# Kernel tuning notes

Measured on AMD Instinct MI355X. Metric: run time of the kernel, lower is better.

## Reference

```python
import jax, jax.numpy as jnp
import numpy as np

B, N, D, K = 4, 2048, 128, 32
EPS = 1e-5  # nn.LayerNorm default eps


def _lin(k, fan_in, fan_out):
    kw, kb = jax.random.split(k)
    s = 1.0 / np.sqrt(fan_in)
    w = jax.random.uniform(kw, (fan_in, fan_out), jnp.float32, -s, s)
    b = jax.random.uniform(kb, (fan_out,), jnp.float32, -s, s)
    return w, b


def setup_inputs() -> dict:
    key = jax.random.key(0)
    ks = jax.random.split(key, 3)
    inp = {}
    inp["features"] = jax.random.normal(ks[0], (B, N, D), jnp.float32)
    inp["coords"] = jax.random.uniform(ks[1], (B, N, 3), jnp.float32) * 64.0
    names = [("ql", D, D), ("kl", D, D), ("vl", D, D), ("pl1", 3, D), ("pl2", D, D),
             ("we1", D, D), ("we2", D, D), ("pe1", 3, D), ("pe2", D, D),
             ("sg1", D, D), ("sg2", D, D)]
    k2 = jax.random.split(ks[2], len(names))
    for (nm, fi, fo), kk in zip(names, k2):
        w, b = _lin(kk, fi, fo)
        inp[nm + "_w"] = w
        inp[nm + "_b"] = b
    inp["lnA_g"] = jnp.ones((D,), jnp.float32)
    inp["lnA_b"] = jnp.zeros((D,), jnp.float32)
    inp["lnF_g"] = jnp.ones((D,), jnp.float32)
    inp["lnF_b"] = jnp.zeros((D,), jnp.float32)
    return inp


def _sparsemax_k(z):
    # sparsemax over axis=1 (the K neighbor axis) of [N, K, D]
    zs = -jnp.sort(-z, axis=1)                      # descending sort
    zc = jnp.cumsum(zs, axis=1)
    r = jnp.arange(1, K + 1, dtype=z.dtype)[None, :, None]
    support = (r * zs) > (zc - 1.0)
    kz = jnp.sum(support, axis=1, keepdims=True).astype(jnp.int32)  # >= 1
    tau = (jnp.take_along_axis(zc, kz - 1, axis=1) - 1.0) / kz.astype(z.dtype)
    return jnp.maximum(z - tau, 0.0)


def _sg_prop(x, src, tgt, n):
    # SGConv (K=1) propagation: D^{-1/2}(A+I)D^{-1/2} x with self-loops added
    ar = jnp.arange(n)
    s = jnp.concatenate([src, ar])
    t = jnp.concatenate([tgt, ar])
    deg = jax.ops.segment_sum(jnp.ones(s.shape, x.dtype), t, num_segments=n)
    dinv = jax.lax.rsqrt(deg)
    norm = dinv[s] * dinv[t]
    return jax.ops.segment_sum(x[s] * norm[:, None], t, num_segments=n)


def reference(features, coords,
              ql_w, ql_b, kl_w, kl_b, vl_w, vl_b,
              pl1_w, pl1_b, pl2_w, pl2_b,
              we1_w, we1_b, we2_w, we2_b,
              lnA_g, lnA_b,
              pe1_w, pe1_b, pe2_w, pe2_b,
              sg1_w, sg1_b, sg2_w, sg2_b,
              lnF_g, lnF_b):
    def ln(x, g, b):
        m = jnp.mean(x, axis=-1, keepdims=True)
        v = jnp.var(x, axis=-1, keepdims=True)
        return (x - m) * jax.lax.rsqrt(v + EPS) * g + b

    def one(feat, coord):
        # ---- RNSA: KNN self-attention with positional embedding ----
        d2 = jnp.sum((coord[:, None, :] - coord[None, :, :]) ** 2, axis=-1)  # [N,N]
        _, idx = jax.lax.top_k(-d2, K)                   # [N,K], self included first
        diff = coord[idx] - coord[:, None, :]            # [N,K,3]
        fc = jnp.maximum(diff @ pl1_w + pl1_b, 0.0) @ pl2_w + pl2_b  # [N,K,D]
        pe = fc + feat[idx]
        Q = jnp.maximum(feat @ ql_w + ql_b, 0.0)         # [N,D]
        Kf = jnp.maximum(pe @ kl_w + kl_b, 0.0)          # [N,K,D]
        V = pe @ vl_w + vl_b
        rel = (Kf - Q[:, None, :]) * fc
        w = jnp.maximum(rel @ we1_w + we1_b, 0.0) @ we2_w + we2_b
        w = _sparsemax_k(w)                              # attn_drop is identity (eval)
        x_att = feat + jnp.einsum('nkd,nkd->nd', V, w)   # residual add
        cf = jnp.maximum(coord @ pe1_w + pe1_b, 0.0) @ pe2_w + pe2_b
        x_in = ln(x_att, lnA_g, lnA_b)
        x_pe = x_in + cf
        d2m = d2 + jnp.where(jnp.eye(N, dtype=bool), jnp.inf, 0.0)  # knn_graph: loop=False
        _, idx2 = jax.lax.top_k(-d2m, K)                 # [N,K] neighbors (sources)
        src = idx2.reshape(-1)
        tgt = jnp.repeat(jnp.arange(N), K)
        h = _sg_prop(x_pe, src, tgt, N) @ sg1_w + sg1_b
        h = jnp.maximum(h, 0.0)
        h = _sg_prop(h, src, tgt, N) @ sg2_w + sg2_b     # dropout is identity (eval)
        return ln(h + x_in, lnF_g, lnF_b)

    return jax.vmap(one)(features, coords)
```

## Files before the change

### kernel.cpp

```cpp
#include <hip/hip_runtime.h>
#include <hip/hip_bf16.h>


namespace {
constexpr int BB = 4;
constexpr int NN = 2048;
constexpr int DD = 128;
constexpr int KK = 32;
constexpr float LNEPS = 1e-5f;
constexpr int SH = 136;
constexpr int SF = 132;

constexpr int W_QL = 0, W_KL = 16384, W_VL = 32768, W_PL2 = 49152, W_WE1 = 65536,
              W_WE2 = 81920, W_PE2 = 98304, W_SG1 = 114688, W_SG2 = 131072,
              W_PL1 = 147456, W_PE1 = 147840,
              B_QL = 148224, B_KL = 148352, B_VL = 148480, B_PL1 = 148608, B_PL2 = 148736,
              B_WE1 = 148864, B_WE2 = 148992, B_PE1 = 149120, B_PE2 = 149248,
              B_SG1 = 149376, B_SG2 = 149504,
              LNA_G = 149632, LNA_B = 149760, LNF_G = 149888, LNF_B = 150016;

constexpr long OFF_FEAT  = 0;
constexpr long OFF_Q     = 1l << 20;
constexpr long OFF_XATT  = 2l << 20;
constexpr long OFF_XIN   = 3l << 20;
constexpr long OFF_XPE   = 4l << 20;
constexpr long OFF_H1    = 5l << 20;
constexpr long OFF_COORD = 6l << 20;
constexpr long OFF_W     = (6l << 20) + 32768;
constexpr long OFF_IDX   = (6l << 20) + 262144;
}

typedef _Float16 f16;
typedef __attribute__((ext_vector_type(8))) _Float16 half8;
typedef __attribute__((ext_vector_type(4))) float f32x4;

struct WPtrs { const void* p[26]; };

__device__ __forceinline__ f32x4 mfma16h(half8 a, half8 b, f32x4 c) {
  return __builtin_amdgcn_mfma_f32_16x16x32_f16(a, b, c, 0, 0, 0);
}
__device__ __forceinline__ bool bf_inputs(const unsigned* __restrict__ dt) {
  return (dt[0] & 0xFFFFu) != 0u;
}

__global__ __launch_bounds__(256) void k_prep(WPtrs wp,
    const void* __restrict__ feat, const void* __restrict__ coord,
    const unsigned* __restrict__ dt,
    float* __restrict__ featf, float* __restrict__ coordf, float* __restrict__ Wf,
    f16* __restrict__ pkH, f16* __restrict__ pkL) {
  const bool isbf = bf_inputs(dt);
  const int tid = threadIdx.x;
  if (blockIdx.x < 2048) {
    const int nf = BB * NN * DD, nc = BB * NN * 3;
    for (int i = blockIdx.x * 256 + tid; i < nf + nc; i += 2048 * 256) {
      if (i < nf) {
        featf[i] = isbf ? __bfloat162float(((const __hip_bfloat16*)feat)[i])
                        : ((const float*)feat)[i];
      } else {
        const int j = i - nf;
        coordf[j] = isbf ? __bfloat162float(((const __hip_bfloat16*)coord)[j])
                         : ((const float*)coord)[j];
      }
    }
  } else if (blockIdx.x < 2048 + 26) {
    const int sizes[26] = {16384,16384,16384,16384,16384,16384,16384,16384,16384,
                           384,384,
                           128,128,128,128,128,128,128,128,128,128,128,
                           128,128,128,128};
    const int offs[26] = {W_QL,W_KL,W_VL,W_PL2,W_WE1,W_WE2,W_PE2,W_SG1,W_SG2,
                          W_PL1,W_PE1,
                          B_QL,B_KL,B_VL,B_PL1,B_PL2,B_WE1,B_WE2,B_PE1,B_PE2,B_SG1,B_SG2,
                          LNA_G,LNA_B,LNF_G,LNF_B};
    const int t = blockIdx.x - 2048;
    float* dst = Wf + offs[t];
    const int n = sizes[t];
    if (isbf) {
      const __hip_bfloat16* src = (const __hip_bfloat16*)wp.p[t];
      for (int i = tid; i < n; i += 256) dst[i] = __bfloat162float(src[i]);
    } else {
      const float* src = (const float*)wp.p[t];
      for (int i = tid; i < n; i += 256) dst[i] = src[i];
    }
  } else {
    const int wmap[9] = {3, 1, 2, 4, 5, 6, 7, 8, 0};
    const int m = blockIdx.x - 2048 - 26;
    const void* src = wp.p[wmap[m]];
    f16* H = pkH + m * 16384;
    f16* L = pkL + m * 16384;
    for (int f = tid; f < 16384; f += 256) {
      const int j = f & 7, lane = (f >> 3) & 63, ks = (f >> 9) & 3, nt = f >> 11;
      const int k = ks * 32 + ((lane >> 4) << 3) + j, n = nt * 16 + (lane & 15);
      const float v = isbf ? __bfloat162float(((const __hip_bfloat16*)src)[k * 128 + n])
                           : ((const float*)src)[k * 128 + n];
      const f16 h = (f16)v;
      H[f] = h;
      L[f] = (f16)(v - (float)h);
    }
  }
}

__device__ __forceinline__ void mm_core(const f16* sA,
                                        const f16* __restrict__ wH,
                                        const f16* __restrict__ wL,
                                        bool useLoW, int lane, int wv, f32x4 acc[2][2]) {
  const int colq = lane & 15, quad = lane >> 4;
  #pragma unroll
  for (int mt = 0; mt < 2; ++mt) {
    const int arow = mt * 16 + colq;
    f32x4 a0 = {0.f, 0.f, 0.f, 0.f}, a1 = {0.f, 0.f, 0.f, 0.f};
    #pragma unroll
    for (int ks = 0; ks < 4; ++ks) {
      const half8 a = *(const half8*)(sA + arow * SH + ks * 32 + quad * 8);
      const int nt0 = 2 * wv, nt1 = 2 * wv + 1;
      const half8 b0 = *(const half8*)(wH + ((nt0 * 4 + ks) * 64 + lane) * 8);
      const half8 b1 = *(const half8*)(wH + ((nt1 * 4 + ks) * 64 + lane) * 8);
      a0 = mfma16h(a, b0, a0);
      a1 = mfma16h(a, b1, a1);
      if (useLoW) {
        const half8 bl0 = *(const half8*)(wL + ((nt0 * 4 + ks) * 64 + lane) * 8);
        const half8 bl1 = *(const half8*)(wL + ((nt1 * 4 + ks) * 64 + lane) * 8);
        a0 = mfma16h(a, bl0, a0);
        a1 = mfma16h(a, bl1, a1);
      }
    }
    acc[mt][0] = a0;
    acc[mt][1] = a1;
  }
}

__device__ __forceinline__ void h_store2(f16* A, int row0, int col, float v0, float v1) {
  A[row0 * SH + col] = (f16)v0;
  A[(row0 + 1) * SH + col] = (f16)v1;
}

__device__ __forceinline__ void h_store_row16(f16* A, int row, int c0, const float* v) {
  half8 o0, o1;
  #pragma unroll
  for (int e = 0; e < 8; ++e) { o0[e] = (f16)v[e]; o1[e] = (f16)v[8 + e]; }
  *(half8*)(A + row * SH + c0) = o0;
  *(half8*)(A + row * SH + c0 + 8) = o1;
}

__global__ __launch_bounds__(256) void k_knn_q(const float* __restrict__ coordf,
                                               const float* __restrict__ featf,
                                               const float* __restrict__ Wf,
                                               const f16* __restrict__ pkH,
                                               const f16* __restrict__ pkL,
                                               const unsigned* __restrict__ dt,
                                               int* __restrict__ idx1, int* __restrict__ idx2,
                                               float* __restrict__ Qm) {
  __shared__ __align__(16) unsigned char smem[NN * 3 * 4 + 4 * 33 * 4];
  const int tid = threadIdx.x;
  if (blockIdx.x < 2048) {
    float* cs = (float*)smem;
    int (*tops)[33] = (int(*)[33])(smem + NN * 3 * 4);
    const int wv = tid >> 6, lane = tid & 63;
    const int blk = blockIdx.x;
    const int b = blk >> 9;
    const int i = ((blk & 511) << 2) + wv;
    const float* cb = coordf + (long)b * NN * 3;
    for (int t = tid; t < NN * 3 / 4; t += 256) ((float4*)cs)[t] = ((const float4*)cb)[t];
    __syncthreads();
    const float qx = cs[i*3+0], qy = cs[i*3+1], qz = cs[i*3+2];
    float v[32];
    unsigned removed = 0u;
    float bv = 1e30f; int bj = 0x7fffffff;
    #pragma unroll
    for (int m = 0; m < 32; m++) {
      const int j = m * 64 + lane;
      const float dx = cs[j*3+0] - qx, dy = cs[j*3+1] - qy, dz = cs[j*3+2] - qz;
      const float d2 = __fadd_rn(__fadd_rn(__fmul_rn(dx,dx), __fmul_rn(dy,dy)), __fmul_rn(dz,dz));
      v[m] = d2;
      if (d2 < bv) { bv = d2; bj = j; }
    }
    for (int s = 0; s < 33; s++) {
      float mv = bv; int mj = bj;
      #pragma unroll
      for (int off = 1; off < 64; off <<= 1) {
        const float ov = __shfl_xor(mv, off, 64);
        const int   oj = __shfl_xor(mj, off, 64);
        if (ov < mv || (ov == mv && oj < mj)) { mv = ov; mj = oj; }
      }
      if (lane == 0) tops[wv][s] = mj;
      if ((mj & 63) == lane) {
        removed |= 1u << (mj >> 6);
        bv = 1e30f; bj = 0x7fffffff;
        #pragma unroll
        for (int m = 0; m < 32; m++) {
          if (!((removed >> m) & 1u) && v[m] < bv) { bv = v[m]; bj = m * 64 + lane; }
        }
      }
    }
    const unsigned long long sm = __ballot(lane < 33 && tops[wv][lane] == i);
    const int p = sm ? (__ffsll((long long)sm) - 1) : 32;
    if (lane < KK) {
      const long g = (long)b * NN + i;
      idx1[g * KK + lane] = tops[wv][lane];
      idx2[g * KK + lane] = tops[wv][lane + (lane >= p ? 1 : 0)];
    }
  } else {
    f16* AH = (f16*)smem;
    const int lane = tid & 63, wv = tid >> 6;
    const int colq = lane & 15, quad = lane >> 4;
    const bool useLoW = !bf_inputs(dt);
    const int row8 = tid >> 3, c0 = (tid & 7) * 16;
    const long gg0 = (long)(blockIdx.x - 2048) * 32;
    float s[16];
    const float* sp = featf + (gg0 + row8) * DD + c0;
    #pragma unroll
    for (int e = 0; e < 16; e += 4) {
      const float4 vv = *(const float4*)(sp + e);
      s[e] = vv.x; s[e+1] = vv.y; s[e+2] = vv.z; s[e+3] = vv.w;
    }
    h_store_row16(AH, row8, c0, s);
    __syncthreads();
    f32x4 acc[2][2];
    mm_core(AH, pkH + 8*16384, pkL + 8*16384, useLoW, lane, wv, acc);
    #pragma unroll
    for (int ntl = 0; ntl < 2; ++ntl) {
      const int col = (2*wv + ntl)*16 + colq;
      const float bv = Wf[B_QL + col];
      #pragma unroll
      for (int mt = 0; mt < 2; ++mt) {
        const int rowb = mt*16 + quad*4;
        #pragma unroll
        for (int r = 0; r < 4; ++r)
          Qm[(gg0 + rowb + r) * DD + col] = fmaxf(acc[mt][ntl][r] + bv, 0.f);
      }
    }
  }
}

__global__ __launch_bounds__(256, 4) void k_attn(const float* __restrict__ featf,
                                              const float* __restrict__ coordf,
                                              const float* __restrict__ Qm,
                                              const int* __restrict__ idx1,
                                              const float* __restrict__ Wf,
                                              const f16* __restrict__ pkH,
                                              const f16* __restrict__ pkL,
                                              const unsigned* __restrict__ dt,
                                              float* __restrict__ x_att) {
  __shared__ __align__(16) f16 AH[KK*SH], CH[KK*SH];
  __shared__ int nb[KK];
  const int tid = threadIdx.x;
  const int lane = tid & 63, wv = tid >> 6;
  const int colq = lane & 15, quad = lane >> 4;
  const int g = blockIdx.x; const int i = g & (NN - 1); const int b = g >> 11;
  const long bN = (long)b * NN;
  const bool useLoW = !bf_inputs(dt);
  if (tid < KK) nb[tid] = idx1[(long)g * KK + tid];
  const int row8 = tid >> 3, c0 = (tid & 7) * 16;

  {
    const int j = idx1[(long)g * KK + row8];
    const float* cb = coordf + (long)b * NN * 3;
    const float dx = cb[j*3+0] - cb[i*3+0], dy = cb[j*3+1] - cb[i*3+1], dz = cb[j*3+2] - cb[i*3+2];
    float t1v[16];
    #pragma unroll
    for (int c4 = 0; c4 < 4; ++c4) {
      const int cc = c0 + c4*4;
      const float4 w0 = *(const float4*)(Wf + W_PL1 + cc);
      const float4 w1 = *(const float4*)(Wf + W_PL1 + 128 + cc);
      const float4 w2 = *(const float4*)(Wf + W_PL1 + 256 + cc);
      const float4 bp = *(const float4*)(Wf + B_PL1 + cc);
      t1v[c4*4+0] = fmaxf(fmaf(dz,w2.x,fmaf(dy,w1.x,fmaf(dx,w0.x,bp.x))), 0.f);
      t1v[c4*4+1] = fmaxf(fmaf(dz,w2.y,fmaf(dy,w1.y,fmaf(dx,w0.y,bp.y))), 0.f);
      t1v[c4*4+2] = fmaxf(fmaf(dz,w2.z,fmaf(dy,w1.z,fmaf(dx,w0.z,bp.z))), 0.f);
      t1v[c4*4+3] = fmaxf(fmaf(dz,w2.w,fmaf(dy,w1.w,fmaf(dx,w0.w,bp.w))), 0.f);
    }
    h_store_row16(AH, row8, c0, t1v);
  }
  __syncthreads();
  f32x4 acc[2][2];
  float fc[2][2][4];
  {
    mm_core(AH, pkH + 0*16384, pkL + 0*16384, useLoW, lane, wv, acc);
    #pragma unroll
    for (int ntl = 0; ntl < 2; ++ntl) {
      const int col = (2*wv + ntl)*16 + colq;
      const float bv = Wf[B_PL2 + col];
      #pragma unroll
      for (int mt = 0; mt < 2; ++mt) {
        const int rowb = mt*16 + quad*4;
        float pe[4];
        #pragma unroll
        for (int r = 0; r < 4; ++r) {
          const float f = acc[mt][ntl][r] + bv;
          fc[mt][ntl][r] = f;
          pe[r] = f + featf[(bN + nb[rowb + r]) * DD + col];
        }
        h_store2(CH, rowb + 0, col, pe[0], pe[1]);
        h_store2(CH, rowb + 2, col, pe[2], pe[3]);
      }
    }
  }
  __syncthreads();
  {
    mm_core(CH, pkH + 1*16384, pkL + 1*16384, useLoW, lane, wv, acc);
    #pragma unroll
    for (int ntl = 0; ntl < 2; ++ntl) {
      const int col = (2*wv + ntl)*16 + colq;
      const float bv = Wf[B_KL + col];
      const float qv = Qm[(bN + i) * DD + col];
      #pragma unroll
      for (int mt = 0; mt < 2; ++mt) {
        const int rowb = mt*16 + quad*4;
        float rel[4];
        #pragma unroll
        for (int r = 0; r < 4; ++r) {
          const float kf = fmaxf(acc[mt][ntl][r] + bv, 0.f);
          rel[r] = (kf - qv) * fc[mt][ntl][r];
        }
        h_store2(AH, rowb + 0, col, rel[0], rel[1]);
        h_store2(AH, rowb + 2, col, rel[2], rel[3]);
      }
    }
  }
  f32x4 Vacc[2][2];
  mm_core(CH, pkH + 2*16384, pkL + 2*16384, useLoW, lane, wv, Vacc);
  __syncthreads();
  {
    mm_core(AH, pkH + 3*16384, pkL + 3*16384, useLoW, lane, wv, acc);
    #pragma unroll
    for (int ntl = 0; ntl < 2; ++ntl) {
      const int col = (2*wv + ntl)*16 + colq;
      const float bv = Wf[B_WE1 + col];
      #pragma unroll
      for (int mt = 0; mt < 2; ++mt) {
        const int rowb = mt*16 + quad*4;
        h_store2(CH, rowb + 0, col,
                 fmaxf(acc[mt][ntl][0] + bv, 0.f), fmaxf(acc[mt][ntl][1] + bv, 0.f));
        h_store2(CH, rowb + 2, col,
                 fmaxf(acc[mt][ntl][2] + bv, 0.f), fmaxf(acc[mt][ntl][3] + bv, 0.f));
      }
    }
  }
  __syncthreads();
  f32x4 Wacc[2][2];
  mm_core(CH, pkH + 4*16384, pkL + 4*16384, useLoW, lane, wv, Wacc);

  #pragma unroll
  for (int ntl = 0; ntl < 2; ++ntl) {
    const int col = (2*wv + ntl)*16 + colq;
    const float bw = Wf[B_WE2 + col];
    const float bvv = Wf[B_VL + col];
    float z[8], Vv[8];
    #pragma unroll
    for (int mt = 0; mt < 2; ++mt)
      #pragma unroll
      for (int r = 0; r < 4; ++r) {
        z[mt*4+r]  = Wacc[mt][ntl][r] + bw;
        Vv[mt*4+r] = Vacc[mt][ntl][r] + bvv;
      }
    float S = 0.f;
    #pragma unroll
    for (int e = 0; e < 8; ++e) S += z[e];
    S += __shfl_xor(S, 16, 64); S += __shfl_xor(S, 32, 64);
    float tau = (S - 1.0f) * (1.0f / 32.0f);
    int cnt = 32;
    for (int it = 0; it < 40; ++it) {
      float s = 0.f; int c = 0;
      #pragma unroll
      for (int e = 0; e < 8; ++e) { if (z[e] > tau) { s += z[e]; c++; } }
      s += __shfl_xor(s, 16, 64); s += __shfl_xor(s, 32, 64);
      c += __shfl_xor(c, 16, 64); c += __shfl_xor(c, 32, 64);
      const float ntau = (s - 1.0f) / (float)c;
      const int changed = (c != cnt);
      cnt = c; tau = ntau;
      if (!__any(changed)) break;
    }
    float pv = 0.f;
    #pragma unroll
    for (int e = 0; e < 8; ++e) pv = fmaf(fmaxf(z[e] - tau, 0.f), Vv[e], pv);
    pv += __shfl_xor(pv, 16, 64); pv += __shfl_xor(pv, 32, 64);
    if (quad == 0) x_att[(bN + i) * DD + col] = featf[(bN + i) * DD + col] + pv;
  }
}

__global__ __launch_bounds__(256) void k_lnA_pe(const float* __restrict__ x_att,
                                                const float* __restrict__ coordf,
                                                const float* __restrict__ Wf,
                                                const f16* __restrict__ pkH,
                                                const f16* __restrict__ pkL,
                                                const unsigned* __restrict__ dt,
                                                float* __restrict__ x_in, float* __restrict__ x_pe) {
  __shared__ __align__(16) f16 AH[KK*SH];
  __shared__ float Xf[KK][SF];
  const int tid = threadIdx.x;
  const int lane = tid & 63, wv = tid >> 6;
  const int colq = lane & 15, quad = lane >> 4;
  const bool useLoW = !bf_inputs(dt);
  const int row8 = tid >> 3, c0 = (tid & 7) * 16;
  const long gg0 = (long)blockIdx.x * 32;
  const long gr = gg0 + row8;
  const int b = (int)(gr >> 11), i = (int)(gr & (NN - 1));

  float xa[16];
  {
    const float* xr = x_att + gr * DD + c0;
    #pragma unroll
    for (int e = 0; e < 16; e += 4) {
      const float4 v = *(const float4*)(xr + e);
      xa[e] = v.x; xa[e+1] = v.y; xa[e+2] = v.z; xa[e+3] = v.w;
    }
  }
  float sm = 0.f, s2 = 0.f;
  #pragma unroll
  for (int e = 0; e < 16; ++e) { sm += xa[e]; s2 = fmaf(xa[e], xa[e], s2); }
  #pragma unroll
  for (int off = 1; off < 8; off <<= 1) {
    sm += __shfl_xor(sm, off, 64);
    s2 += __shfl_xor(s2, off, 64);
  }
  const float m = sm * (1.f/128.f);
  const float var = s2 * (1.f/128.f) - m * m;
  const float rstd = rsqrtf(var + LNEPS);
  float xin[16];
  #pragma unroll
  for (int e = 0; e < 16; ++e) {
    xin[e] = (xa[e] - m) * rstd * Wf[LNA_G + c0 + e] + Wf[LNA_B + c0 + e];
    Xf[row8][c0 + e] = xin[e];
  }
  #pragma unroll
  for (int e = 0; e < 16; e += 4) {
    float4 v; v.x = xin[e]; v.y = xin[e+1]; v.z = xin[e+2]; v.w = xin[e+3];
    *(float4*)(x_in + gr * DD + c0 + e) = v;
  }
  {
    const float* cp = coordf + ((long)b * NN + i) * 3;
    const float cx = cp[0], cy = cp[1], cz = cp[2];
    float tv[16];
    #pragma unroll
    for (int c4 = 0; c4 < 4; ++c4) {
      const int cc = c0 + c4*4;
      const float4 w0 = *(const float4*)(Wf + W_PE1 + cc);
      const float4 w1 = *(const float4*)(Wf + W_PE1 + 128 + cc);
      const float4 w2 = *(const float4*)(Wf + W_PE1 + 256 + cc);
      const float4 bp = *(const float4*)(Wf + B_PE1 + cc);
      tv[c4*4+0] = fmaxf(fmaf(cz,w2.x,fmaf(cy,w1.x,fmaf(cx,w0.x,bp.x))), 0.f);
      tv[c4*4+1] = fmaxf(fmaf(cz,w2.y,fmaf(cy,w1.y,fmaf(cx,w0.y,bp.y))), 0.f);
      tv[c4*4+2] = fmaxf(fmaf(cz,w2.z,fmaf(cy,w1.z,fmaf(cx,w0.z,bp.z))), 0.f);
      tv[c4*4+3] = fmaxf(fmaf(cz,w2.w,fmaf(cy,w1.w,fmaf(cx,w0.w,bp.w))), 0.f);
    }
    h_store_row16(AH, row8, c0, tv);
  }
  __syncthreads();
  f32x4 acc[2][2];
  mm_core(AH, pkH + 5*16384, pkL + 5*16384, useLoW, lane, wv, acc);
  #pragma unroll
  for (int ntl = 0; ntl < 2; ++ntl) {
    const int col = (2*wv + ntl)*16 + colq;
    const float bv = Wf[B_PE2 + col];
    #pragma unroll
    for (int mt = 0; mt < 2; ++mt) {
      const int rowb = mt*16 + quad*4;
      #pragma unroll
      for (int r = 0; r < 4; ++r)
        x_pe[(gg0 + rowb + r) * DD + col] = Xf[rowb + r][col] + acc[mt][ntl][r] + bv;
    }
  }
}

__global__ __launch_bounds__(256) void k_sg1(const float* __restrict__ x_pe,
                                             const int* __restrict__ idx2,
                                             const float* __restrict__ Wf,
                                             const f16* __restrict__ pkH,
                                             const f16* __restrict__ pkL,
                                             const unsigned* __restrict__ dt,
                                             float* __restrict__ h1) {
  __shared__ __align__(16) f16 AH[KK*SH];
  __shared__ int nb2[32][KK];
  const int tid = threadIdx.x;
  const int lane = tid & 63, wv = tid >> 6;
  const int colq = lane & 15, quad = lane >> 4;
  const bool useLoW = !bf_inputs(dt);
  const int row8 = tid >> 3, c0 = (tid & 7) * 16;
  const long gg0 = (long)blockIdx.x * 32;
  const long bN = (gg0 >> 11) << 11;
  for (int t = tid; t < 32 * KK; t += 256)
    nb2[t >> 5][t & 31] = idx2[(gg0 + (t >> 5)) * KK + (t & 31)];
  __syncthreads();
  float s[16];
  {
    const float* sp = x_pe + (gg0 + row8) * DD + c0;
    #pragma unroll
    for (int e = 0; e < 16; e += 4) {
      const float4 v = *(const float4*)(sp + e);
      s[e] = v.x; s[e+1] = v.y; s[e+2] = v.z; s[e+3] = v.w;
    }
  }
  for (int k = 0; k < KK; ++k) {
    const float* np_ = x_pe + (bN + nb2[row8][k]) * DD + c0;
    #pragma unroll
    for (int e = 0; e < 16; e += 4) {
      const float4 v = *(const float4*)(np_ + e);
      s[e] += v.x; s[e+1] += v.y; s[e+2] += v.z; s[e+3] += v.w;
    }
  }
  #pragma unroll
  for (int e = 0; e < 16; ++e) s[e] *= (1.f / 33.f);
  h_store_row16(AH, row8, c0, s);
  __syncthreads();
  f32x4 acc[2][2];
  mm_core(AH, pkH + 6*16384, pkL + 6*16384, useLoW, lane, wv, acc);
  #pragma unroll
  for (int ntl = 0; ntl < 2; ++ntl) {
    const int col = (2*wv + ntl)*16 + colq;
    const float bv = Wf[B_SG1 + col];
    #pragma unroll
    for (int mt = 0; mt < 2; ++mt) {
      const int rowb = mt*16 + quad*4;
      #pragma unroll
      for (int r = 0; r < 4; ++r)
        h1[(gg0 + rowb + r) * DD + col] = fmaxf(acc[mt][ntl][r] + bv, 0.f);
    }
  }
}

__global__ __launch_bounds__(256) void k_sg2(const float* __restrict__ h1,
                                             const int* __restrict__ idx2,
                                             const float* __restrict__ x_in,
                                             const float* __restrict__ Wf,
                                             const f16* __restrict__ pkH,
                                             const f16* __restrict__ pkL,
                                             const unsigned* __restrict__ dt,
                                             void* __restrict__ out) {
  __shared__ __align__(16) f16 AH[KK*SH];
  __shared__ float Yf[KK][SF];
  __shared__ int nb2[32][KK];
  const int tid = threadIdx.x;
  const int lane = tid & 63, wv = tid >> 6;
  const int colq = lane & 15, quad = lane >> 4;
  const bool isbf = bf_inputs(dt);
  const bool useLoW = !isbf;
  const int row8 = tid >> 3, c0 = (tid & 7) * 16;
  const long gg0 = (long)blockIdx.x * 32;
  const long bN = (gg0 >> 11) << 11;
  for (int t = tid; t < 32 * KK; t += 256)
    nb2[t >> 5][t & 31] = idx2[(gg0 + (t >> 5)) * KK + (t & 31)];
  __syncthreads();
  float s[16];
  {
    const float* sp = h1 + (gg0 + row8) * DD + c0;
    #pragma unroll
    for (int e = 0; e < 16; e += 4) {
      const float4 v = *(const float4*)(sp + e);
      s[e] = v.x; s[e+1] = v.y; s[e+2] = v.z; s[e+3] = v.w;
    }
  }
  for (int k = 0; k < KK; ++k) {
    const float* np_ = h1 + (bN + nb2[row8][k]) * DD + c0;
    #pragma unroll
    for (int e = 0; e < 16; e += 4) {
      const float4 v = *(const float4*)(np_ + e);
      s[e] += v.x; s[e+1] += v.y; s[e+2] += v.z; s[e+3] += v.w;
    }
  }
  #pragma unroll
  for (int e = 0; e < 16; ++e) s[e] *= (1.f / 33.f);
  h_store_row16(AH, row8, c0, s);
  __syncthreads();
  f32x4 acc[2][2];
  mm_core(AH, pkH + 7*16384, pkL + 7*16384, useLoW, lane, wv, acc);
  #pragma unroll
  for (int ntl = 0; ntl < 2; ++ntl) {
    const int col = (2*wv + ntl)*16 + colq;
    const float bv = Wf[B_SG2 + col];
    #pragma unroll
    for (int mt = 0; mt < 2; ++mt) {
      const int rowb = mt*16 + quad*4;
      #pragma unroll
      for (int r = 0; r < 4; ++r)
        Yf[rowb + r][col] = acc[mt][ntl][r] + bv + x_in[(gg0 + rowb + r) * DD + col];
    }
  }
  __syncthreads();
  float y[16];
  #pragma unroll
  for (int e = 0; e < 16; ++e) y[e] = Yf[row8][c0 + e];
  float sm = 0.f, s2 = 0.f;
  #pragma unroll
  for (int e = 0; e < 16; ++e) { sm += y[e]; s2 = fmaf(y[e], y[e], s2); }
  #pragma unroll
  for (int off = 1; off < 8; off <<= 1) {
    sm += __shfl_xor(sm, off, 64);
    s2 += __shfl_xor(s2, off, 64);
  }
  const float m = sm * (1.f/128.f);
  const float var = s2 * (1.f/128.f) - m * m;
  const float rstd = rsqrtf(var + LNEPS);
  const long gr = gg0 + row8;
  #pragma unroll
  for (int e = 0; e < 16; ++e) {
    const float o = (y[e] - m) * rstd * Wf[LNF_G + c0 + e] + Wf[LNF_B + c0 + e];
    if (isbf) ((__hip_bfloat16*)out)[gr * DD + c0 + e] = __float2bfloat16(o);
    else      ((float*)out)[gr * DD + c0 + e] = o;
  }
}

extern "C" void kernel_launch(void* const* d_in, const int* in_sizes, int n_in,
                              void* d_out, int out_size, void* d_ws, size_t ws_size,
                              hipStream_t stream) {
  float* ws = (float*)d_ws;
  float* featf  = ws + OFF_FEAT;
  float* Qm     = ws + OFF_Q;
  float* x_att  = ws + OFF_XATT;
  float* x_in   = ws + OFF_XIN;
  float* x_pe   = ws + OFF_XPE;
  float* h1     = ws + OFF_H1;
  float* coordf = ws + OFF_COORD;
  float* Wf     = ws + OFF_W;
  int* idx1 = (int*)(ws + OFF_IDX);
  int* idx2 = idx1 + (long)BB * NN * KK;
  f16* pkH = (f16*)(idx2 + (long)BB * NN * KK);
  f16* pkL = pkH + 9 * 16384;
  const unsigned* dt = (const unsigned*)d_in[24];

  WPtrs wp;
  const int map[26] = {2,4,6,10,12,14,18,20,22, 8,16,
                       3,5,7,9,11,13,15,17,19,21,23,
                       24,25,26,27};
  for (int t = 0; t < 26; t++) wp.p[t] = d_in[map[t]];

  k_prep<<<2048 + 26 + 9, 256, 0, stream>>>(wp, d_in[0], d_in[1], dt,
                                            featf, coordf, Wf, pkH, pkL);
  k_knn_q<<<BB * NN / 4 + BB * NN / 32, 256, 0, stream>>>(coordf, featf, Wf, pkH, pkL, dt,
                                                          idx1, idx2, Qm);
  k_attn<<<BB * NN, 256, 0, stream>>>(featf, coordf, Qm, idx1, Wf, pkH, pkL, dt, x_att);
  k_lnA_pe<<<BB * NN / 32, 256, 0, stream>>>(x_att, coordf, Wf, pkH, pkL, dt, x_in, x_pe);
  k_sg1<<<BB * NN / 32, 256, 0, stream>>>(x_pe, idx2, Wf, pkH, pkL, dt, h1);
  k_sg2<<<BB * NN / 32, 256, 0, stream>>>(h1, idx2, x_in, Wf, pkH, pkL, dt, (void*)d_out);
}
```

Baseline: 477.8 us.

## Process two query points per attention block with 64-row MFMA tiles

The attention kernel now handles two points per workgroup, stacking their 32 neighbor rows into 64-row tiles. A new mm_core64 reuses each loaded weight fragment across four M-tiles instead of two, which halves weight-fragment traffic per point and halves the grid size. In exchange it doubles shared memory and accumulator registers per block, which may lower occupancy under the 256x4 launch bound.

```diff
diff --git a/kernel.cpp b/kernel.cpp
--- a/kernel.cpp
+++ b/kernel.cpp
@@ -111,6 +111,35 @@
     #pragma unroll
     for (int ks = 0; ks < 4; ++ks) {
       const half8 a = *(const half8*)(sA + arow * SH + ks * 32 + quad * 8);
+      const int nt0 = 2 * wv, nt1 = 2 * wv + 1;
+      const half8 b0 = *(const half8*)(wH + ((nt0 * 4 + ks) * 64 + lane) * 8);
+      const half8 b1 = *(const half8*)(wH + ((nt1 * 4 + ks) * 64 + lane) * 8);
+      a0 = mfma16h(a, b0, a0);
+      a1 = mfma16h(a, b1, a1);
+      if (useLoW) {
+        const half8 bl0 = *(const half8*)(wL + ((nt0 * 4 + ks) * 64 + lane) * 8);
+        const half8 bl1 = *(const half8*)(wL + ((nt1 * 4 + ks) * 64 + lane) * 8);
+        a0 = mfma16h(a, bl0, a0);
+        a1 = mfma16h(a, bl1, a1);
+      }
+    }
+    acc[mt][0] = a0;
+    acc[mt][1] = a1;
+  }
+}
+
+__device__ __forceinline__ void mm_core64(const f16* sA,
+                                          const f16* __restrict__ wH,
+                                          const f16* __restrict__ wL,
+                                          bool useLoW, int lane, int wv, f32x4 acc[4][2]) {
+  const int colq = lane & 15;
+  #pragma unroll
+  for (int mt = 0; mt < 4; ++mt) {
+    const int arow = mt * 16 + colq;
+    f32x4 a0 = {0.f, 0.f, 0.f, 0.f}, a1 = {0.f, 0.f, 0.f, 0.f};
+    #pragma unroll
+    for (int ks = 0; ks < 4; ++ks) {
+      const half8 a = *(const half8*)(sA + arow * SH + ks * 32 + (lane >> 4) * 8);
       const int nt0 = 2 * wv, nt1 = 2 * wv + 1;
       const half8 b0 = *(const half8*)(wH + ((nt0 * 4 + ks) * 64 + lane) * 8);
       const half8 b1 = *(const half8*)(wH + ((nt1 * 4 + ks) * 64 + lane) * 8);
@@ -240,47 +269,52 @@
                                               const f16* __restrict__ pkL,
                                               const unsigned* __restrict__ dt,
                                               float* __restrict__ x_att) {
-  __shared__ __align__(16) f16 AH[KK*SH], CH[KK*SH];
-  __shared__ int nb[KK];
+  __shared__ __align__(16) f16 AH[2*KK*SH], CH[2*KK*SH];
+  __shared__ int nb[2*KK];
   const int tid = threadIdx.x;
   const int lane = tid & 63, wv = tid >> 6;
   const int colq = lane & 15, quad = lane >> 4;
-  const int g = blockIdx.x; const int i = g & (NN - 1); const int b = g >> 11;
+  const long g0 = (long)blockIdx.x * 2;
+  const int i0 = (int)(g0 & (NN - 1)); const int b = (int)(g0 >> 11);
   const long bN = (long)b * NN;
   const bool useLoW = !bf_inputs(dt);
-  if (tid < KK) nb[tid] = idx1[(long)g * KK + tid];
+  if (tid < 2*KK) nb[tid] = idx1[(g0 + (tid >> 5)) * KK + (tid & 31)];
   const int row8 = tid >> 3, c0 = (tid & 7) * 16;
 
   {
-    const int j = idx1[(long)g * KK + row8];
     const float* cb = coordf + (long)b * NN * 3;
-    const float dx = cb[j*3+0] - cb[i*3+0], dy = cb[j*3+1] - cb[i*3+1], dz = cb[j*3+2] - cb[i*3+2];
-    float t1v[16];
-    #pragma unroll
-    for (int c4 = 0; c4 < 4; ++c4) {
-      const int cc = c0 + c4*4;
-      const float4 w0 = *(const float4*)(Wf + W_PL1 + cc);
-      const float4 w1 = *(const float4*)(Wf + W_PL1 + 128 + cc);
-      const float4 w2 = *(const float4*)(Wf + W_PL1 + 256 + cc);
-      const float4 bp = *(const float4*)(Wf + B_PL1 + cc);
-      t1v[c4*4+0] = fmaxf(fmaf(dz,w2.x,fmaf(dy,w1.x,fmaf(dx,w0.x,bp.x))), 0.f);
-      t1v[c4*4+1] = fmaxf(fmaf(dz,w2.y,fmaf(dy,w1.y,fmaf(dx,w0.y,bp.y))), 0.f);
-      t1v[c4*4+2] = fmaxf(fmaf(dz,w2.z,fmaf(dy,w1.z,fmaf(dx,w0.z,bp.z))), 0.f);
-      t1v[c4*4+3] = fmaxf(fmaf(dz,w2.w,fmaf(dy,w1.w,fmaf(dx,w0.w,bp.w))), 0.f);
-    }
-    h_store_row16(AH, row8, c0, t1v);
-  }
-  __syncthreads();
-  f32x4 acc[2][2];
-  float fc[2][2][4];
-  {
-    mm_core(AH, pkH + 0*16384, pkL + 0*16384, useLoW, lane, wv, acc);
+    #pragma unroll
+    for (int pp = 0; pp < 2; ++pp) {
+      const int ip = i0 + pp;
+      const int j = idx1[(g0 + pp) * KK + row8];
+      const float dx = cb[j*3+0] - cb[ip*3+0], dy = cb[j*3+1] - cb[ip*3+1], dz = cb[j*3+2] - cb[ip*3+2];
+      float t1v[16];
+      #pragma unroll
+      for (int c4 = 0; c4 < 4; ++c4) {
+        const int cc = c0 + c4*4;
+        const float4 w0 = *(const float4*)(Wf + W_PL1 + cc);
+        const float4 w1 = *(const float4*)(Wf + W_PL1 + 128 + cc);
+        const float4 w2 = *(const float4*)(Wf + W_PL1 + 256 + cc);
+        const float4 bp = *(const float4*)(Wf + B_PL1 + cc);
+        t1v[c4*4+0] = fmaxf(fmaf(dz,w2.x,fmaf(dy,w1.x,fmaf(dx,w0.x,bp.x))), 0.f);
+        t1v[c4*4+1] = fmaxf(fmaf(dz,w2.y,fmaf(dy,w1.y,fmaf(dx,w0.y,bp.y))), 0.f);
+        t1v[c4*4+2] = fmaxf(fmaf(dz,w2.z,fmaf(dy,w1.z,fmaf(dx,w0.z,bp.z))), 0.f);
+        t1v[c4*4+3] = fmaxf(fmaf(dz,w2.w,fmaf(dy,w1.w,fmaf(dx,w0.w,bp.w))), 0.f);
+      }
+      h_store_row16(AH, pp * KK + row8, c0, t1v);
+    }
+  }
+  __syncthreads();
+  f32x4 acc[4][2];
+  float fc[4][2][4];
+  {
+    mm_core64(AH, pkH + 0*16384, pkL + 0*16384, useLoW, lane, wv, acc);
     #pragma unroll
     for (int ntl = 0; ntl < 2; ++ntl) {
       const int col = (2*wv + ntl)*16 + colq;
       const float bv = Wf[B_PL2 + col];
       #pragma unroll
-      for (int mt = 0; mt < 2; ++mt) {
+      for (int mt = 0; mt < 4; ++mt) {
         const int rowb = mt*16 + quad*4;
         float pe[4];
         #pragma unroll
@@ -296,15 +330,17 @@
   }
   __syncthreads();
   {
-    mm_core(CH, pkH + 1*16384, pkL + 1*16384, useLoW, lane, wv, acc);
+    mm_core64(CH, pkH + 1*16384, pkL + 1*16384, useLoW, lane, wv, acc);
     #pragma unroll
     for (int ntl = 0; ntl < 2; ++ntl) {
       const int col = (2*wv + ntl)*16 + colq;
       const float bv = Wf[B_KL + col];
-      const float qv = Qm[(bN + i) * DD + col];
-      #pragma unroll
-      for (int mt = 0; mt < 2; ++mt) {
+      const float qv0 = Qm[(bN + i0) * DD + col];
+      const float qv1 = Qm[(bN + i0 + 1) * DD + col];
+      #pragma unroll
+      for (int mt = 0; mt < 4; ++mt) {
         const int rowb = mt*16 + quad*4;
+        const float qv = (mt < 2) ? qv0 : qv1;
         float rel[4];
         #pragma unroll
         for (int r = 0; r < 4; ++r) {
@@ -316,17 +352,17 @@
       }
     }
   }
-  f32x4 Vacc[2][2];
-  mm_core(CH, pkH + 2*16384, pkL + 2*16384, useLoW, lane, wv, Vacc);
-  __syncthreads();
-  {
-    mm_core(AH, pkH + 3*16384, pkL + 3*16384, useLoW, lane, wv, acc);
+  f32x4 Vacc[4][2];
+  mm_core64(CH, pkH + 2*16384, pkL + 2*16384, useLoW, lane, wv, Vacc);
+  __syncthreads();
+  {
+    mm_core64(AH, pkH + 3*16384, pkL + 3*16384, useLoW, lane, wv, acc);
     #pragma unroll
     for (int ntl = 0; ntl < 2; ++ntl) {
       const int col = (2*wv + ntl)*16 + colq;
       const float bv = Wf[B_WE1 + col];
       #pragma unroll
-      for (int mt = 0; mt < 2; ++mt) {
+      for (int mt = 0; mt < 4; ++mt) {
         const int rowb = mt*16 + quad*4;
         h_store2(CH, rowb + 0, col,
                  fmaxf(acc[mt][ntl][0] + bv, 0.f), fmaxf(acc[mt][ntl][1] + bv, 0.f));
@@ -336,44 +372,50 @@
     }
   }
   __syncthreads();
-  f32x4 Wacc[2][2];
-  mm_core(CH, pkH + 4*16384, pkL + 4*16384, useLoW, lane, wv, Wacc);
-
-  #pragma unroll
-  for (int ntl = 0; ntl < 2; ++ntl) {
-    const int col = (2*wv + ntl)*16 + colq;
-    const float bw = Wf[B_WE2 + col];
-    const float bvv = Wf[B_VL + col];
-    float z[8], Vv[8];
-    #pragma unroll
-    for (int mt = 0; mt < 2; ++mt)
-      #pragma unroll
-      for (int r = 0; r < 4; ++r) {
-        z[mt*4+r]  = Wacc[mt][ntl][r] + bw;
-        Vv[mt*4+r] = Vacc[mt][ntl][r] + bvv;
-      }
-    float S = 0.f;
-    #pragma unroll
-    for (int e = 0; e < 8; ++e) S += z[e];
-    S += __shfl_xor(S, 16, 64); S += __shfl_xor(S, 32, 64);
-    float tau = (S - 1.0f) * (1.0f / 32.0f);
-    int cnt = 32;
-    for (int it = 0; it < 40; ++it) {
-      float s = 0.f; int c = 0;
-      #pragma unroll
-      for (int e = 0; e < 8; ++e) { if (z[e] > tau) { s += z[e]; c++; } }
-      s += __shfl_xor(s, 16, 64); s += __shfl_xor(s, 32, 64);
-      c += __shfl_xor(c, 16, 64); c += __shfl_xor(c, 32, 64);
-      const float ntau = (s - 1.0f) / (float)c;
-      const int changed = (c != cnt);
-      cnt = c; tau = ntau;
-      if (!__any(changed)) break;
-    }
-    float pv = 0.f;
-    #pragma unroll
-    for (int e = 0; e < 8; ++e) pv = fmaf(fmaxf(z[e] - tau, 0.f), Vv[e], pv);
-    pv += __shfl_xor(pv, 16, 64); pv += __shfl_xor(pv, 32, 64);
-    if (quad == 0) x_att[(bN + i) * DD + col] = featf[(bN + i) * DD + col] + pv;
+  f32x4 Wacc[4][2];
+  mm_core64(CH, pkH + 4*16384, pkL + 4*16384, useLoW, lane, wv, Wacc);
+
+  #pragma unroll
+  for (int pp = 0; pp < 2; ++pp) {
+    #pragma unroll
+    for (int ntl = 0; ntl < 2; ++ntl) {
+      const int col = (2*wv + ntl)*16 + colq;
+      const float bw = Wf[B_WE2 + col];
+      const float bvv = Wf[B_VL + col];
+      float z[8], Vv[8];
+      #pragma unroll
+      for (int m2 = 0; m2 < 2; ++m2)
+        #pragma unroll
+        for (int r = 0; r < 4; ++r) {
+          z[m2*4+r]  = Wacc[2*pp + m2][ntl][r] + bw;
+          Vv[m2*4+r] = Vacc[2*pp + m2][ntl][r] + bvv;
+        }
+      float S = 0.f;
+      #pragma unroll
+      for (int e = 0; e < 8; ++e) S += z[e];
+      S += __shfl_xor(S, 16, 64); S += __shfl_xor(S, 32, 64);
+      float tau = (S - 1.0f) * (1.0f / 32.0f);
+      int cnt = 32;
+      for (int it = 0; it < 40; ++it) {
+        float s = 0.f; int c = 0;
+        #pragma unroll
+        for (int e = 0; e < 8; ++e) { if (z[e] > tau) { s += z[e]; c++; } }
+        s += __shfl_xor(s, 16, 64); s += __shfl_xor(s, 32, 64);
+        c += __shfl_xor(c, 16, 64); c += __shfl_xor(c, 32, 64);
+        const float ntau = (s - 1.0f) / (float)c;
+        const int changed = (c != cnt);
+        cnt = c; tau = ntau;
+        if (!__any(changed)) break;
+      }
+      float pv = 0.f;
+      #pragma unroll
+      for (int e = 0; e < 8; ++e) pv = fmaf(fmaxf(z[e] - tau, 0.f), Vv[e], pv);
+      pv += __shfl_xor(pv, 16, 64); pv += __shfl_xor(pv, 32, 64);
+      if (quad == 0) {
+        const long gi = bN + i0 + pp;
+        x_att[gi * DD + col] = featf[gi * DD + col] + pv;
+      }
+    }
   }
 }
 
@@ -626,7 +668,7 @@
                                             featf, coordf, Wf, pkH, pkL);
   k_knn_q<<<BB * NN / 4 + BB * NN / 32, 256, 0, stream>>>(coordf, featf, Wf, pkH, pkL, dt,
                                                           idx1, idx2, Qm);
-  k_attn<<<BB * NN, 256, 0, stream>>>(featf, coordf, Qm, idx1, Wf, pkH, pkL, dt, x_att);
+  k_attn<<<BB * NN / 2, 256, 0, stream>>>(featf, coordf, Qm, idx1, Wf, pkH, pkL, dt, x_att);
   k_lnA_pe<<<BB * NN / 32, 256, 0, stream>>>(x_att, coordf, Wf, pkH, pkL, dt, x_in, x_pe);
   k_sg1<<<BB * NN / 32, 256, 0, stream>>>(x_pe, idx2, Wf, pkH, pkL, dt, h1);
   k_sg2<<<BB * NN / 32, 256, 0, stream>>>(h1, idx2, x_in, Wf, pkH, pkL, dt, (void*)d_out);
```

Result: slower. 570.1 us (+19.3%).
